# Kernel optimization log

Measured on AMD Instinct MI355X. Metric: run time of the kernel, lower is better.

Reference implementation:

```python
import jax, jax.numpy as jnp
import numpy as np

N = 100000   # nodes
E = 1600000  # edges
F = 128      # input features
H = 128      # hidden
O = 64       # output classes
BN_EPS = 1e-5


def gcn_conv(x, edge_index, W, b, n_nodes):
    """PyG-style GCNConv: h = D^-1/2 (A+I) D^-1/2 (x W) + b."""
    h = x @ W  # [N, out]
    row = jnp.concatenate([edge_index[0], jnp.arange(n_nodes)])  # add self loops
    col = jnp.concatenate([edge_index[1], jnp.arange(n_nodes)])
    deg = jax.ops.segment_sum(jnp.ones_like(row, dtype=h.dtype), row, num_segments=n_nodes)
    dinv = jnp.where(deg > 0, jax.lax.rsqrt(deg), 0.0)
    norm = dinv[row] * dinv[col]                 # [E+N]
    msg = h[col] * norm[:, None]                 # gather + scale
    out = jax.ops.segment_sum(msg, row, num_segments=n_nodes)  # scatter-add
    return out + b


def batch_norm(x, gamma, beta):
    mean = jnp.mean(x, axis=0)
    var = jnp.var(x, axis=0)
    return (x - mean) * jax.lax.rsqrt(var + BN_EPS) * gamma + beta


def setup_inputs() -> dict:
    key = jax.random.key(0)
    ks = jax.random.split(key, 10)
    x = jax.random.normal(ks[0], (N, F), dtype=jnp.float32)
    edge_index = jax.random.randint(ks[1], (2, E), 0, N, dtype=jnp.int64)
    W1 = jax.random.normal(ks[2], (F, H), dtype=jnp.float32) / np.sqrt(F)
    b1 = jnp.zeros((H,), dtype=jnp.float32)
    gamma1 = jnp.ones((H,), dtype=jnp.float32)
    beta1 = jnp.zeros((H,), dtype=jnp.float32)
    W2 = jax.random.normal(ks[3], (H, H), dtype=jnp.float32) / np.sqrt(H)
    b2 = jnp.zeros((H,), dtype=jnp.float32)
    W3 = jax.random.normal(ks[4], (H, O), dtype=jnp.float32) / np.sqrt(H)
    b3 = jnp.zeros((O,), dtype=jnp.float32)
    return {"x": x, "edge_index": edge_index, "W1": W1, "b1": b1,
            "gamma1": gamma1, "beta1": beta1, "W2": W2, "b2": b2,
            "W3": W3, "b3": b3}


def reference(x, edge_index, W1, b1, gamma1, beta1, W2, b2, W3, b3):
    h = gcn_conv(x, edge_index, W1, b1, N)
    h = jax.nn.relu(batch_norm(h, gamma1, beta1))
    h = gcn_conv(h, edge_index, W2, b2, N)
    h = jax.nn.relu(h)
    out = h @ W3 + b3  # final Linear classifier head [N, O]
    return out
```

## Files before the change

kernel.cpp:

```cpp
#include <hip/hip_runtime.h>

#define NN 100000
#define EE 1600000
#define HN 128
#define OO 64
#define SB 256
#define NBUCK 196
#define CH 4096

typedef __attribute__((ext_vector_type(8))) short bf16x8;
typedef __attribute__((ext_vector_type(4))) float f32x4;

__device__ __forceinline__ unsigned short f2bf(float f){
  unsigned u = __float_as_uint(f);
  return (unsigned short)((u + 0x7FFFu + ((u >> 16) & 1u)) >> 16);
}
__device__ __forceinline__ float bflo(unsigned u){ return __uint_as_float(u << 16); }
__device__ __forceinline__ float bfhi(unsigned u){ return __uint_as_float(u & 0xFFFF0000u); }

__global__ __launch_bounds__(256) void k_histpack(const int* __restrict__ rows, int* __restrict__ bcnt,
                                                  const float* __restrict__ W1, const float* __restrict__ W2,
                                                  const float* __restrict__ W3,
                                                  unsigned short* __restrict__ Wp1, unsigned short* __restrict__ Wp2,
                                                  unsigned short* __restrict__ Wp3){
  __shared__ int h[NBUCK];
  for (int i = threadIdx.x; i < NBUCK; i += 256) h[i] = 0;
  __syncthreads();
  int base = blockIdx.x * CH;
  for (int j = threadIdx.x; j < CH; j += 256){
    int e = base + j;
    if (e < EE) atomicAdd(&h[rows[e] >> 9], 1);
  }
  __syncthreads();
  for (int i = threadIdx.x; i < NBUCK; i += 256){
    int v = h[i];
    if (v) atomicAdd(&bcnt[i], v);
  }
  int b = blockIdx.x;
  if (b < 20){
    const float* W; unsigned short* Wp; int outc, i0;
    if (b < 8)      { W=W1; Wp=Wp1; outc=128; i0 = b*256; }
    else if (b < 16){ W=W2; Wp=Wp2; outc=128; i0 = (b-8)*256; }
    else            { W=W3; Wp=Wp3; outc=64;  i0 = (b-16)*256; }
    int i = i0 + threadIdx.x;
    if (i < 16*outc){
      int kb = i / outc, n = i - kb*outc;
      unsigned pk[4];
      #pragma unroll
      for (int jj = 0; jj < 4; ++jj){
        unsigned lo = f2bf(W[(size_t)(kb*8 + 2*jj)*outc + n]);
        unsigned hi = f2bf(W[(size_t)(kb*8 + 2*jj+1)*outc + n]);
        pk[jj] = lo | (hi << 16);
      }
      *reinterpret_cast<uint4*>(Wp + (size_t)i*8) = make_uint4(pk[0],pk[1],pk[2],pk[3]);
    }
  }
}

__global__ __launch_bounds__(64) void k_bscan(const int* __restrict__ bcnt,
                                              int* __restrict__ bbase, int* __restrict__ bcur){
  int lane = threadIdx.x;
  int run = 0;
  for (int c = 0; c < NBUCK; c += 64){
    int i = c + lane;
    int v = (i < NBUCK) ? bcnt[i] : 0;
    int s = v;
    #pragma unroll
    for (int d = 1; d < 64; d <<= 1){ int u = __shfl_up(s, d); if (lane >= d) s += u; }
    if (i < NBUCK){ bbase[i] = run + s - v; bcur[i] = run + s - v; }
    run += __shfl(s, 63);
  }
}

__global__ __launch_bounds__(256) void k_bucket(const int* __restrict__ rows, const int* __restrict__ cols,
                                                int* __restrict__ bcur, uint2* __restrict__ ebuf){
  __shared__ int bc[NBUCK];
  __shared__ int boff[NBUCK];
  __shared__ int ccur[NBUCK];
  __shared__ int gbase[NBUCK];
  __shared__ uint2 stage[CH];
  const int t = threadIdx.x;
  const int base = blockIdx.x * CH;
  const int nval = min(CH, EE - base);

  for (int i = t; i < NBUCK; i += 256) bc[i] = 0;
  __syncthreads();

  int er[16], ec[16];
  #pragma unroll
  for (int j = 0; j < 16; ++j){
    int i = j*256 + t;
    if (i < nval){
      er[j] = rows[base+i]; ec[j] = cols[base+i];
      atomicAdd(&bc[er[j] >> 9], 1);
    } else er[j] = -1;
  }
  __syncthreads();

  if (t < 64){
    int lane = t, run = 0;
    for (int c = 0; c < NBUCK; c += 64){
      int i = c + lane;
      int v = (i < NBUCK) ? bc[i] : 0;
      int s = v;
      #pragma unroll
      for (int d = 1; d < 64; d <<= 1){ int u = __shfl_up(s, d); if (lane >= d) s += u; }
      if (i < NBUCK) boff[i] = run + s - v;
      run += __shfl(s, 63);
    }
  }
  __syncthreads();
  if (t < NBUCK){
    gbase[t] = bc[t] ? atomicAdd(&bcur[t], bc[t]) : 0;
    ccur[t]  = boff[t];
  }
  __syncthreads();
  #pragma unroll
  for (int j = 0; j < 16; ++j){
    if (er[j] >= 0){
      int b = er[j] >> 9;
      int p = atomicAdd(&ccur[b], 1);
      stage[p] = make_uint2((unsigned)er[j], (unsigned)ec[j]);
    }
  }
  __syncthreads();
  for (int i = t; i < nval; i += 256){
    uint2 e = stage[i];
    int b = (int)(e.x >> 9);
    ebuf[gbase[b] + (i - boff[b])] = e;
  }
}

__global__ __launch_bounds__(256) void k_build(const uint2* __restrict__ ebuf,
                                               const int* __restrict__ bbase, const int* __restrict__ bcnt,
                                               int* __restrict__ row_start, int* __restrict__ cnt,
                                               float* __restrict__ dinv, int* __restrict__ csr_col){
  __shared__ int hist[512];
  __shared__ int cur[512];
  const int b = blockIdx.x;
  const int row0 = b << 9;
  const int nrow = min(512, NN - row0);
  const int ebase = bbase[b];
  const int ne = bcnt[b];
  const int t = threadIdx.x;

  for (int i = t; i < nrow; i += 256) hist[i] = 0;
  __syncthreads();
  for (int i = t; i < ne; i += 256)
    atomicAdd(&hist[(int)ebuf[ebase+i].x - row0], 1);
  __syncthreads();

  if (t < 64){
    int lane = t, run = 0;
    for (int c = 0; c < nrow; c += 64){
      int i = c + lane;
      int v = (i < nrow) ? hist[i] : 0;
      int s = v;
      #pragma unroll
      for (int d = 1; d < 64; d <<= 1){ int u = __shfl_up(s, d); if (lane >= d) s += u; }
      if (i < nrow) cur[i] = run + s - v;
      run += __shfl(s, 63);
    }
  }
  __syncthreads();
  for (int i = t; i < nrow; i += 256){
    int h = hist[i];
    int r = row0 + i;
    cnt[r] = h;
    dinv[r] = rsqrtf((float)(h+1));
    row_start[r] = ebase + cur[i];
    cur[i] += ebase;
  }
  __syncthreads();
  for (int i = t; i < ne; i += 256){
    uint2 e = ebuf[ebase+i];
    int p = atomicAdd(&cur[(int)e.x - row0], 1);
    csr_col[p] = (int)e.y;
  }
}

template<bool BF16OUT>
__global__ __launch_bounds__(256) void k_agg(const unsigned* __restrict__ h,
                                             const int* __restrict__ row_start,
                                             const int* __restrict__ cnt,
                                             const int* __restrict__ col,
                                             const float* __restrict__ dinv,
                                             const float* __restrict__ bias,
                                             void* __restrict__ outv){
  int wib  = __builtin_amdgcn_readfirstlane((int)(threadIdx.x >> 6));
  int wid  = blockIdx.x*4 + wib;
  int lane = threadIdx.x & 63;
  if (wid >= NN) return;
  int s = row_start[wid];
  int e = s + cnt[wid];
  float dr = dinv[wid];
  const unsigned* hp = h + lane;
  float ax, ay;
  {
    unsigned u = hp[(size_t)wid*64];
    ax = bflo(u); ay = bfhi(u);
  }
  int p = s;
  for (; p+7 < e; p += 8){
    unsigned uu[8];
    #pragma unroll
    for (int j=0;j<8;++j) uu[j] = hp[(size_t)col[p+j]*64];
    #pragma unroll
    for (int j=0;j<8;++j){ ax += bflo(uu[j]); ay += bfhi(uu[j]); }
  }
  for (; p+3 < e; p += 4){
    unsigned uu[4];
    #pragma unroll
    for (int j=0;j<4;++j) uu[j] = hp[(size_t)col[p+j]*64];
    #pragma unroll
    for (int j=0;j<4;++j){ ax += bflo(uu[j]); ay += bfhi(uu[j]); }
  }
  for (; p < e; ++p){
    unsigned u = hp[(size_t)col[p]*64];
    ax += bflo(u); ay += bfhi(u);
  }
  float2 bb = *reinterpret_cast<const float2*>(bias + 2*lane);
  float ox = ax*dr + bb.x, oy = ay*dr + bb.y;
  if constexpr (BF16OUT){
    ((unsigned*)outv)[(size_t)wid*64 + lane] = (unsigned)f2bf(ox) | ((unsigned)f2bf(oy) << 16);
  } else {
    *reinterpret_cast<float2*>((float*)outv + (size_t)wid*HN + 2*lane) = make_float2(ox, oy);
  }
}

template<int OUTC, int XFORM, bool ADD_BIAS, bool BF16OUT, bool ABF16>
__global__ __launch_bounds__(256) void k_mgemm(const void* __restrict__ Av,
                                               const unsigned short* __restrict__ Wp,
                                               const float* __restrict__ scale,
                                               const float* __restrict__ shiftv,
                                               const float* __restrict__ bias,
                                               const float* __restrict__ dinv,
                                               void* __restrict__ Cv){
  __shared__ char AsB[32768];
  const int t = threadIdx.x;
  const int row0 = blockIdx.x * 128;

  if constexpr (ABF16){
    const uint4* A = (const uint4*)Av;
    const int c8 = t & 15;
    const int k0 = c8*8;
    float sc[8], sh[8];
    if (XFORM == 1){
      #pragma unroll
      for (int j=0;j<8;++j){ sc[j]=scale[k0+j]; sh[j]=shiftv[k0+j]; }
    }
    #pragma unroll
    for (int g = 0; g < 8; ++g){
      int f = g*256 + t;
      int r = f >> 4;
      int row = row0 + r;
      int rc = row < NN ? row : NN-1;
      uint4 q = A[(size_t)rc*16 + c8];
      float vf[8] = { bflo(q.x),bfhi(q.x),bflo(q.y),bfhi(q.y),
                      bflo(q.z),bfhi(q.z),bflo(q.w),bfhi(q.w) };
      if (XFORM == 1){
        #pragma unroll
        for (int j=0;j<8;++j) vf[j] = fmaxf(fmaf(vf[j], sc[j], sh[j]), 0.f);
      } else if (XFORM == 2){
        #pragma unroll
        for (int j=0;j<8;++j) vf[j] = fmaxf(vf[j], 0.f);
      }
      unsigned pk[4];
      #pragma unroll
      for (int j=0;j<4;++j)
        pk[j] = (unsigned)f2bf(vf[2*j]) | ((unsigned)f2bf(vf[2*j+1]) << 16);
      int boff = (c8*16) ^ ((r & 7) << 4);
      *reinterpret_cast<uint4*>(AsB + r*256 + boff) = make_uint4(pk[0],pk[1],pk[2],pk[3]);
    }
  } else {
    const float* A = (const float*)Av;
    #pragma unroll
    for (int g = 0; g < 16; ++g){
      int f = g*256 + t;
      int r = f >> 5;
      int c4 = f & 31;
      int row = row0 + r;
      int rc = row < NN ? row : NN-1;
      float4 v = *reinterpret_cast<const float4*>(A + (size_t)rc*HN + c4*4);
      if (XFORM == 2){
        v.x = fmaxf(v.x, 0.f); v.y = fmaxf(v.y, 0.f);
        v.z = fmaxf(v.z, 0.f); v.w = fmaxf(v.w, 0.f);
      }
      unsigned p0 = (unsigned)f2bf(v.x) | ((unsigned)f2bf(v.y) << 16);
      unsigned p1 = (unsigned)f2bf(v.z) | ((unsigned)f2bf(v.w) << 16);
      int boff = (c4*8) ^ ((r & 7) << 4);
      *reinterpret_cast<uint2*>(AsB + r*256 + boff) = make_uint2(p0, p1);
    }
  }
  __syncthreads();

  const int wv = t >> 6;
  const int l  = t & 63;
  const int lm = l & 15;
  const int lk = l >> 4;
  constexpr int NF = OUTC/16;

  f32x4 acc[2][NF];
  #pragma unroll
  for (int mi=0;mi<2;++mi)
    #pragma unroll
    for (int ni=0;ni<NF;++ni) acc[mi][ni] = (f32x4){0.f,0.f,0.f,0.f};

  const bf16x8* WpV = reinterpret_cast<const bf16x8*>(Wp);

  #pragma unroll
  for (int ks = 0; ks < 4; ++ks){
    bf16x8 af[2];
    #pragma unroll
    for (int mi=0;mi<2;++mi){
      int R = wv*32 + mi*16 + lm;
      int boff = (ks*64 + lk*16) ^ ((R & 7) << 4);
      af[mi] = *reinterpret_cast<const bf16x8*>(AsB + R*256 + boff);
    }
    int kb = ks*4 + lk;
    #pragma unroll
    for (int ni=0;ni<NF;++ni){
      int n = ni*16 + lm;
      bf16x8 bfr = WpV[kb*OUTC + n];
      acc[0][ni] = __builtin_amdgcn_mfma_f32_16x16x32_bf16(af[0], bfr, acc[0][ni], 0,0,0);
      acc[1][ni] = __builtin_amdgcn_mfma_f32_16x16x32_bf16(af[1], bfr, acc[1][ni], 0,0,0);
    }
  }

  #pragma unroll
  for (int mi=0;mi<2;++mi){
    #pragma unroll
    for (int j=0;j<4;++j){
      int grow = row0 + wv*32 + mi*16 + lk*4 + j;
      if (grow >= NN) continue;
      if constexpr (BF16OUT){
        float dr = dinv[grow];
        unsigned short* po = (unsigned short*)Cv + (size_t)grow*OUTC;
        #pragma unroll
        for (int ni=0;ni<NF;++ni)
          po[ni*16 + lm] = f2bf(acc[mi][ni][j] * dr);
      } else {
        float* po = (float*)Cv + (size_t)grow*OUTC;
        #pragma unroll
        for (int ni=0;ni<NF;++ni){
          float v = acc[mi][ni][j];
          if (ADD_BIAS) v += bias[ni*16 + lm];
          po[ni*16 + lm] = v;
        }
      }
    }
  }
}

__global__ __launch_bounds__(256) void k_stats(const unsigned* __restrict__ a,
                                               float* __restrict__ ps, float* __restrict__ pq){
  __shared__ float l0[256], l1[256], m0[256], m1[256];
  int c = threadIdx.x & 63;
  int grp = threadIdx.x >> 6;
  float s0=0.f,s1=0.f,q0=0.f,q1=0.f;
  for (int r = blockIdx.x*4 + grp; r < NN; r += SB*4){
    unsigned u = a[(size_t)r*64 + c];
    float v0 = bflo(u), v1 = bfhi(u);
    s0 += v0; s1 += v1; q0 = fmaf(v0,v0,q0); q1 = fmaf(v1,v1,q1);
  }
  l0[threadIdx.x]=s0; l1[threadIdx.x]=s1; m0[threadIdx.x]=q0; m1[threadIdx.x]=q1;
  __syncthreads();
  if (grp==0){
    #pragma unroll
    for (int g=1;g<4;++g){ s0+=l0[g*64+c]; s1+=l1[g*64+c]; q0+=m0[g*64+c]; q1+=m1[g*64+c]; }
    ps[blockIdx.x*128 + 2*c]   = s0; ps[blockIdx.x*128 + 2*c+1] = s1;
    pq[blockIdx.x*128 + 2*c]   = q0; pq[blockIdx.x*128 + 2*c+1] = q1;
  }
}

__global__ __launch_bounds__(128) void k_bnfinal(const float* __restrict__ ps, const float* __restrict__ pq,
                                                 const float* __restrict__ gamma, const float* __restrict__ beta,
                                                 float* __restrict__ scale, float* __restrict__ shiftv){
  int c = threadIdx.x;
  float s=0.f, q=0.f;
  for (int b=0;b<SB;b++){ s += ps[b*128+c]; q += pq[b*128+c]; }
  float mean = s * (1.0f/NN);
  float var  = q * (1.0f/NN) - mean*mean;
  float inv  = rsqrtf(var + 1e-5f);
  float sc = gamma[c]*inv;
  scale[c]  = sc;
  shiftv[c] = beta[c] - mean*sc;
}

extern "C" void kernel_launch(void* const* d_in, const int* in_sizes, int n_in,
                              void* d_out, int out_size, void* d_ws, size_t ws_size,
                              hipStream_t stream) {
  const float* x      = (const float*)d_in[0];
  const int*   ei     = (const int*)d_in[1];
  const int*   rows   = ei;
  const int*   cols   = ei + EE;
  const float* W1     = (const float*)d_in[2];
  const float* b1     = (const float*)d_in[3];
  const float* gamma1 = (const float*)d_in[4];
  const float* beta1  = (const float*)d_in[5];
  const float* W2     = (const float*)d_in[6];
  const float* b2     = (const float*)d_in[7];
  const float* W3     = (const float*)d_in[8];
  const float* b3     = (const float*)d_in[9];
  float* out = (float*)d_out;

  char* w = (char*)d_ws;
  float* buf0      = (float*)w; w += (size_t)NN*HN*4;
  float* buf1      = (float*)w; w += (size_t)NN*HN*4;
  int*   csr_col   = (int*)w;   w += (size_t)EE*4;
  int*   row_start = (int*)w;   w += (size_t)NN*4;
  int*   cnt       = (int*)w;   w += (size_t)NN*4;
  float* dinv      = (float*)w; w += (size_t)NN*4;
  float* ps        = (float*)w; w += (size_t)SB*128*4;
  float* pq        = (float*)w; w += (size_t)SB*128*4;
  float* scale     = (float*)w; w += 1024;
  float* shiftv    = (float*)w; w += 1024;
  int*   bcnt      = (int*)w;   w += 1024;
  int*   bbase     = (int*)w;   w += 1024;
  int*   bcur      = (int*)w;   w += 1024;
  unsigned short* Wp1 = (unsigned short*)w; w += 128*128*2;
  unsigned short* Wp2 = (unsigned short*)w; w += 128*128*2;
  unsigned short* Wp3 = (unsigned short*)w; w += 128*64*2;
  uint2*    ebuf  = (uint2*)buf0;
  unsigned* hbf   = (unsigned*)buf0;
  unsigned* abf   = (unsigned*)buf1;

  (void)hipMemsetAsync(bcnt, 0, NBUCK*4, stream);

  const int CB = (EE + CH - 1)/CH, GB = (NN+127)/128, AB = NN/4;

  k_histpack<<<CB, 256, 0, stream>>>(rows, bcnt, W1, W2, W3, Wp1, Wp2, Wp3);
  k_bscan <<<1, 64, 0, stream>>>(bcnt, bbase, bcur);
  k_bucket<<<CB, 256, 0, stream>>>(rows, cols, bcur, ebuf);
  k_build <<<NBUCK, 256, 0, stream>>>(ebuf, bbase, bcnt, row_start, cnt, dinv, csr_col);

  k_mgemm<128,0,false,true,false><<<GB, 256, 0, stream>>>(x, Wp1, nullptr, nullptr, nullptr, dinv, hbf);
  k_agg<true><<<AB, 256, 0, stream>>>(hbf, row_start, cnt, csr_col, dinv, b1, abf);
  k_stats<<<SB, 256, 0, stream>>>(abf, ps, pq);
  k_bnfinal<<<1, 128, 0, stream>>>(ps, pq, gamma1, beta1, scale, shiftv);

  k_mgemm<128,1,false,true,true><<<GB, 256, 0, stream>>>(abf, Wp2, scale, shiftv, nullptr, dinv, hbf);
  k_agg<true><<<AB, 256, 0, stream>>>(hbf, row_start, cnt, csr_col, dinv, b2, abf);

  k_mgemm<64,2,true,false,true><<<GB, 256, 0, stream>>>(abf, Wp3, nullptr, nullptr, b3, nullptr, out);
}
```

Baseline: 274.1 us.

## Fuse final aggregation with output GEMM and remove small scan/finalize kernels

```diff
diff --git a/kernel.cpp b/kernel.cpp
--- a/kernel.cpp
+++ b/kernel.cpp
@@ -57,25 +57,12 @@
   }
 }
 
-__global__ __launch_bounds__(64) void k_bscan(const int* __restrict__ bcnt,
-                                              int* __restrict__ bbase, int* __restrict__ bcur){
-  int lane = threadIdx.x;
-  int run = 0;
-  for (int c = 0; c < NBUCK; c += 64){
-    int i = c + lane;
-    int v = (i < NBUCK) ? bcnt[i] : 0;
-    int s = v;
-    #pragma unroll
-    for (int d = 1; d < 64; d <<= 1){ int u = __shfl_up(s, d); if (lane >= d) s += u; }
-    if (i < NBUCK){ bbase[i] = run + s - v; bcur[i] = run + s - v; }
-    run += __shfl(s, 63);
-  }
-}
-
 __global__ __launch_bounds__(256) void k_bucket(const int* __restrict__ rows, const int* __restrict__ cols,
-                                                int* __restrict__ bcur, uint2* __restrict__ ebuf){
+                                                const int* __restrict__ bcnt, int* __restrict__ pcur,
+                                                uint2* __restrict__ ebuf){
   __shared__ int bc[NBUCK];
   __shared__ int boff[NBUCK];
+  __shared__ int gBB[NBUCK];
   __shared__ int ccur[NBUCK];
   __shared__ int gbase[NBUCK];
   __shared__ uint2 stage[CH];
@@ -98,20 +85,25 @@
   __syncthreads();
 
   if (t < 64){
-    int lane = t, run = 0;
+    int lane = t, run = 0, grun = 0;
     for (int c = 0; c < NBUCK; c += 64){
       int i = c + lane;
       int v = (i < NBUCK) ? bc[i] : 0;
-      int s = v;
-      #pragma unroll
-      for (int d = 1; d < 64; d <<= 1){ int u = __shfl_up(s, d); if (lane >= d) s += u; }
-      if (i < NBUCK) boff[i] = run + s - v;
+      int g = (i < NBUCK) ? bcnt[i] : 0;
+      int s = v, gs = g;
+      #pragma unroll
+      for (int d = 1; d < 64; d <<= 1){
+        int u = __shfl_up(s, d);  if (lane >= d) s += u;
+        int gu = __shfl_up(gs, d); if (lane >= d) gs += gu;
+      }
+      if (i < NBUCK){ boff[i] = run + s - v; gBB[i] = grun + gs - g; }
       run += __shfl(s, 63);
+      grun += __shfl(gs, 63);
     }
   }
   __syncthreads();
   if (t < NBUCK){
-    gbase[t] = bc[t] ? atomicAdd(&bcur[t], bc[t]) : 0;
+    gbase[t] = bc[t] ? (gBB[t] + atomicAdd(&pcur[t], bc[t])) : 0;
     ccur[t]  = boff[t];
   }
   __syncthreads();
@@ -132,20 +124,28 @@
 }
 
 __global__ __launch_bounds__(256) void k_build(const uint2* __restrict__ ebuf,
-                                               const int* __restrict__ bbase, const int* __restrict__ bcnt,
+                                               const int* __restrict__ bcnt,
                                                int* __restrict__ row_start, int* __restrict__ cnt,
                                                float* __restrict__ dinv, int* __restrict__ csr_col){
   __shared__ int hist[512];
   __shared__ int cur[512];
+  __shared__ int sEbase;
   const int b = blockIdx.x;
   const int row0 = b << 9;
   const int nrow = min(512, NN - row0);
-  const int ebase = bbase[b];
   const int ne = bcnt[b];
   const int t = threadIdx.x;
 
+  if (t < 64){
+    int acc = 0;
+    for (int i = t; i < b; i += 64) acc += bcnt[i];
+    #pragma unroll
+    for (int d = 32; d; d >>= 1) acc += __shfl_xor(acc, d);
+    if (t == 0) sEbase = acc;
+  }
   for (int i = t; i < nrow; i += 256) hist[i] = 0;
   __syncthreads();
+  const int ebase = sEbase;
   for (int i = t; i < ne; i += 256)
     atomicAdd(&hist[(int)ebuf[ebase+i].x - row0], 1);
   __syncthreads();
@@ -179,14 +179,13 @@
   }
 }
 
-template<bool BF16OUT>
 __global__ __launch_bounds__(256) void k_agg(const unsigned* __restrict__ h,
                                              const int* __restrict__ row_start,
                                              const int* __restrict__ cnt,
                                              const int* __restrict__ col,
                                              const float* __restrict__ dinv,
                                              const float* __restrict__ bias,
-                                             void* __restrict__ outv){
+                                             unsigned* __restrict__ outv){
   int wib  = __builtin_amdgcn_readfirstlane((int)(threadIdx.x >> 6));
   int wid  = blockIdx.x*4 + wib;
   int lane = threadIdx.x & 63;
@@ -221,19 +220,97 @@
   }
   float2 bb = *reinterpret_cast<const float2*>(bias + 2*lane);
   float ox = ax*dr + bb.x, oy = ay*dr + bb.y;
-  if constexpr (BF16OUT){
-    ((unsigned*)outv)[(size_t)wid*64 + lane] = (unsigned)f2bf(ox) | ((unsigned)f2bf(oy) << 16);
-  } else {
-    *reinterpret_cast<float2*>((float*)outv + (size_t)wid*HN + 2*lane) = make_float2(ox, oy);
-  }
-}
-
-template<int OUTC, int XFORM, bool ADD_BIAS, bool BF16OUT, bool ABF16>
+  outv[(size_t)wid*64 + lane] = (unsigned)f2bf(ox) | ((unsigned)f2bf(oy) << 16);
+}
+
+__global__ __launch_bounds__(256) void k_aggmm(const unsigned* __restrict__ h,
+                                               const int* __restrict__ row_start,
+                                               const int* __restrict__ cnt,
+                                               const int* __restrict__ col,
+                                               const float* __restrict__ dinv,
+                                               const float* __restrict__ b2,
+                                               const unsigned short* __restrict__ Wp3,
+                                               const float* __restrict__ b3,
+                                               float* __restrict__ out){
+  __shared__ char AsB[32*256];
+  const int t = threadIdx.x;
+  const int wv = __builtin_amdgcn_readfirstlane(t >> 6);
+  const int lane = t & 63;
+  const int tile = blockIdx.x * 32;
+
+  for (int k = 0; k < 8; ++k){
+    int wid = tile + wv*8 + k;
+    int s = row_start[wid];
+    int e = s + cnt[wid];
+    float dr = dinv[wid];
+    const unsigned* hp = h + lane;
+    float ax, ay;
+    { unsigned u = hp[(size_t)wid*64]; ax = bflo(u); ay = bfhi(u); }
+    int p = s;
+    for (; p+7 < e; p += 8){
+      unsigned uu[8];
+      #pragma unroll
+      for (int j=0;j<8;++j) uu[j] = hp[(size_t)col[p+j]*64];
+      #pragma unroll
+      for (int j=0;j<8;++j){ ax += bflo(uu[j]); ay += bfhi(uu[j]); }
+    }
+    for (; p+3 < e; p += 4){
+      unsigned uu[4];
+      #pragma unroll
+      for (int j=0;j<4;++j) uu[j] = hp[(size_t)col[p+j]*64];
+      #pragma unroll
+      for (int j=0;j<4;++j){ ax += bflo(uu[j]); ay += bfhi(uu[j]); }
+    }
+    for (; p < e; ++p){
+      unsigned u = hp[(size_t)col[p]*64];
+      ax += bflo(u); ay += bfhi(u);
+    }
+    float2 bb = *reinterpret_cast<const float2*>(b2 + 2*lane);
+    float ox = fmaxf(ax*dr + bb.x, 0.f);
+    float oy = fmaxf(ay*dr + bb.y, 0.f);
+    int r = wv*8 + k;
+    unsigned pk = (unsigned)f2bf(ox) | ((unsigned)f2bf(oy) << 16);
+    *reinterpret_cast<unsigned*>(AsB + r*256 + ((lane*4) ^ ((r & 7) << 4))) = pk;
+  }
+  __syncthreads();
+
+  const int lm = lane & 15;
+  const int lk = lane >> 4;
+  const int mb  = wv >> 1;
+  const int nb2 = (wv & 1) * 2;
+  f32x4 acc[2] = {(f32x4){0.f,0.f,0.f,0.f},(f32x4){0.f,0.f,0.f,0.f}};
+  const bf16x8* WpV = reinterpret_cast<const bf16x8*>(Wp3);
+
+  #pragma unroll
+  for (int ks = 0; ks < 4; ++ks){
+    int R = mb*16 + lm;
+    bf16x8 af = *reinterpret_cast<const bf16x8*>(AsB + R*256 + ((ks*64 + lk*16) ^ ((R & 7) << 4)));
+    int kb = ks*4 + lk;
+    #pragma unroll
+    for (int ni = 0; ni < 2; ++ni){
+      int n = (nb2+ni)*16 + lm;
+      bf16x8 bfr = WpV[kb*OO + n];
+      acc[ni] = __builtin_amdgcn_mfma_f32_16x16x32_bf16(af, bfr, acc[ni], 0,0,0);
+    }
+  }
+
+  #pragma unroll
+  for (int ni = 0; ni < 2; ++ni){
+    int gcol = (nb2+ni)*16 + lm;
+    float bb = b3[gcol];
+    #pragma unroll
+    for (int j = 0; j < 4; ++j){
+      int grow = tile + mb*16 + lk*4 + j;
+      out[(size_t)grow*OO + gcol] = acc[ni][j] + bb;
+    }
+  }
+}
+
+template<int OUTC, int XFORM, bool BF16OUT, bool ABF16>
 __global__ __launch_bounds__(256) void k_mgemm(const void* __restrict__ Av,
                                                const unsigned short* __restrict__ Wp,
                                                const float* __restrict__ scale,
                                                const float* __restrict__ shiftv,
-                                               const float* __restrict__ bias,
                                                const float* __restrict__ dinv,
                                                void* __restrict__ Cv){
   __shared__ char AsB[32768];
@@ -261,9 +338,6 @@
       if (XFORM == 1){
         #pragma unroll
         for (int j=0;j<8;++j) vf[j] = fmaxf(fmaf(vf[j], sc[j], sh[j]), 0.f);
-      } else if (XFORM == 2){
-        #pragma unroll
-        for (int j=0;j<8;++j) vf[j] = fmaxf(vf[j], 0.f);
       }
       unsigned pk[4];
       #pragma unroll
@@ -282,10 +356,6 @@
       int row = row0 + r;
       int rc = row < NN ? row : NN-1;
       float4 v = *reinterpret_cast<const float4*>(A + (size_t)rc*HN + c4*4);
-      if (XFORM == 2){
-        v.x = fmaxf(v.x, 0.f); v.y = fmaxf(v.y, 0.f);
-        v.z = fmaxf(v.z, 0.f); v.w = fmaxf(v.w, 0.f);
-      }
       unsigned p0 = (unsigned)f2bf(v.x) | ((unsigned)f2bf(v.y) << 16);
       unsigned p1 = (unsigned)f2bf(v.z) | ((unsigned)f2bf(v.w) << 16);
       int boff = (c4*8) ^ ((r & 7) << 4);
@@ -342,19 +412,20 @@
       } else {
         float* po = (float*)Cv + (size_t)grow*OUTC;
         #pragma unroll
-        for (int ni=0;ni<NF;++ni){
-          float v = acc[mi][ni][j];
-          if (ADD_BIAS) v += bias[ni*16 + lm];
-          po[ni*16 + lm] = v;
-        }
+        for (int ni=0;ni<NF;++ni)
+          po[ni*16 + lm] = acc[mi][ni][j];
       }
     }
   }
 }
 
-__global__ __launch_bounds__(256) void k_stats(const unsigned* __restrict__ a,
-                                               float* __restrict__ ps, float* __restrict__ pq){
+__global__ __launch_bounds__(256) void k_statsfin(const unsigned* __restrict__ a,
+                                                  float* __restrict__ ps, float* __restrict__ pq,
+                                                  const float* __restrict__ gamma, const float* __restrict__ beta,
+                                                  float* __restrict__ scale, float* __restrict__ shiftv,
+                                                  int* __restrict__ done){
   __shared__ float l0[256], l1[256], m0[256], m1[256];
+  __shared__ int last;
   int c = threadIdx.x & 63;
   int grp = threadIdx.x >> 6;
   float s0=0.f,s1=0.f,q0=0.f,q1=0.f;
@@ -371,20 +442,20 @@
     ps[blockIdx.x*128 + 2*c]   = s0; ps[blockIdx.x*128 + 2*c+1] = s1;
     pq[blockIdx.x*128 + 2*c]   = q0; pq[blockIdx.x*128 + 2*c+1] = q1;
   }
-}
-
-__global__ __launch_bounds__(128) void k_bnfinal(const float* __restrict__ ps, const float* __restrict__ pq,
-                                                 const float* __restrict__ gamma, const float* __restrict__ beta,
-                                                 float* __restrict__ scale, float* __restrict__ shiftv){
-  int c = threadIdx.x;
-  float s=0.f, q=0.f;
-  for (int b=0;b<SB;b++){ s += ps[b*128+c]; q += pq[b*128+c]; }
-  float mean = s * (1.0f/NN);
-  float var  = q * (1.0f/NN) - mean*mean;
-  float inv  = rsqrtf(var + 1e-5f);
-  float sc = gamma[c]*inv;
-  scale[c]  = sc;
-  shiftv[c] = beta[c] - mean*sc;
+  __threadfence();
+  if (threadIdx.x == 0) last = (atomicAdd(done, 1) == SB-1);
+  __syncthreads();
+  if (last && threadIdx.x < 128){
+    int ch = threadIdx.x;
+    float s=0.f, q=0.f;
+    for (int b=0;b<SB;b++){ s += ps[b*128+ch]; q += pq[b*128+ch]; }
+    float mean = s * (1.0f/NN);
+    float var  = q * (1.0f/NN) - mean*mean;
+    float inv  = rsqrtf(var + 1e-5f);
+    float sc = gamma[ch]*inv;
+    scale[ch]  = sc;
+    shiftv[ch] = beta[ch] - mean*sc;
+  }
 }
 
 extern "C" void kernel_launch(void* const* d_in, const int* in_sizes, int n_in,
@@ -415,32 +486,30 @@
   float* pq        = (float*)w; w += (size_t)SB*128*4;
   float* scale     = (float*)w; w += 1024;
   float* shiftv    = (float*)w; w += 1024;
-  int*   bcnt      = (int*)w;   w += 1024;
-  int*   bbase     = (int*)w;   w += 1024;
-  int*   bcur      = (int*)w;   w += 1024;
+  int*   scr0      = (int*)w;   w += 4096;
   unsigned short* Wp1 = (unsigned short*)w; w += 128*128*2;
   unsigned short* Wp2 = (unsigned short*)w; w += 128*128*2;
   unsigned short* Wp3 = (unsigned short*)w; w += 128*64*2;
+  int* bcnt = scr0;
+  int* pcur = scr0 + 256;
+  int* done = scr0 + 512;
   uint2*    ebuf  = (uint2*)buf0;
   unsigned* hbf   = (unsigned*)buf0;
   unsigned* abf   = (unsigned*)buf1;
 
-  (void)hipMemsetAsync(bcnt, 0, NBUCK*4, stream);
-
-  const int CB = (EE + CH - 1)/CH, GB = (NN+127)/128, AB = NN/4;
+  (void)hipMemsetAsync(scr0, 0, 4096, stream);
+
+  const int CB = (EE + CH - 1)/CH, GB = (NN+127)/128, AB = NN/4, FB = NN/32;
 
   k_histpack<<<CB, 256, 0, stream>>>(rows, bcnt, W1, W2, W3, Wp1, Wp2, Wp3);
-  k_bscan <<<1, 64, 0, stream>>>(bcnt, bbase, bcur);
-  k_bucket<<<CB, 256, 0, stream>>>(rows, cols, bcur, ebuf);
-  k_build <<<NBUCK, 256, 0, stream>>>(ebuf, bbase, bcnt, row_start, cnt, dinv, csr_col);
-
-  k_mgemm<128,0,false,true,false><<<GB, 256, 0, stream>>>(x, Wp1, nullptr, nullptr, nullptr, dinv, hbf);
-  k_agg<true><<<AB, 256, 0, stream>>>(hbf, row_start, cnt, csr_col, dinv, b1, abf);
-  k_stats<<<SB, 256, 0, stream>>>(abf, ps, pq);
-  k_bnfinal<<<1, 128, 0, stream>>>(ps, pq, gamma1, beta1, scale, shiftv);
-
-  k_mgemm<128,1,false,true,true><<<GB, 256, 0, stream>>>(abf, Wp2, scale, shiftv, nullptr, dinv, hbf);
-  k_agg<true><<<AB, 256, 0, stream>>>(hbf, row_start, cnt, csr_col, dinv, b2, abf);
-
-  k_mgemm<64,2,true,false,true><<<GB, 256, 0, stream>>>(abf, Wp3, nullptr, nullptr, b3, nullptr, out);
-}
+  k_bucket  <<<CB, 256, 0, stream>>>(rows, cols, bcnt, pcur, ebuf);
+  k_build   <<<NBUCK, 256, 0, stream>>>(ebuf, bcnt, row_start, cnt, dinv, csr_col);
+
+  k_mgemm<128,0,true,false><<<GB, 256, 0, stream>>>(x, Wp1, nullptr, nullptr, dinv, hbf);
+  k_agg<<<AB, 256, 0, stream>>>(hbf, row_start, cnt, csr_col, dinv, b1, abf);
+  k_statsfin<<<SB, 256, 0, stream>>>(abf, ps, pq, gamma1, beta1, scale, shiftv, done);
+
+  k_mgemm<128,1,true,true><<<GB, 256, 0, stream>>>(abf, Wp2, scale, shiftv, dinv, hbf);
+
+  k_aggmm<<<FB, 256, 0, stream>>>(hbf, row_start, cnt, csr_col, dinv, b2, Wp3, b3, out);
+}
```

New measurement: 278.7 us. About the same (+1.7%).

## Slice features into 16-column slabs for aggregation and drop histogram/scan pre-pass

Applied to the files above, without the earlier changes.

```diff
diff --git a/kernel.cpp b/kernel.cpp
--- a/kernel.cpp
+++ b/kernel.cpp
@@ -7,6 +7,7 @@
 #define SB 256
 #define NBUCK 196
 #define CH 4096
+#define SLAB 16384
 
 typedef __attribute__((ext_vector_type(8))) short bf16x8;
 typedef __attribute__((ext_vector_type(4))) float f32x4;
@@ -17,32 +18,85 @@
 }
 __device__ __forceinline__ float bflo(unsigned u){ return __uint_as_float(u << 16); }
 __device__ __forceinline__ float bfhi(unsigned u){ return __uint_as_float(u & 0xFFFF0000u); }
-
-__global__ __launch_bounds__(256) void k_histpack(const int* __restrict__ rows, int* __restrict__ bcnt,
-                                                  const float* __restrict__ W1, const float* __restrict__ W2,
-                                                  const float* __restrict__ W3,
-                                                  unsigned short* __restrict__ Wp1, unsigned short* __restrict__ Wp2,
-                                                  unsigned short* __restrict__ Wp3){
-  __shared__ int h[NBUCK];
-  for (int i = threadIdx.x; i < NBUCK; i += 256) h[i] = 0;
-  __syncthreads();
-  int base = blockIdx.x * CH;
-  for (int j = threadIdx.x; j < CH; j += 256){
-    int e = base + j;
-    if (e < EE) atomicAdd(&h[rows[e] >> 9], 1);
-  }
-  __syncthreads();
-  for (int i = threadIdx.x; i < NBUCK; i += 256){
-    int v = h[i];
-    if (v) atomicAdd(&bcnt[i], v);
-  }
+__device__ __forceinline__ unsigned bnrelu2(unsigned u, float s0, float h0, float s1, float h1){
+  float v0 = fmaxf(fmaf(bflo(u), s0, h0), 0.f);
+  float v1 = fmaxf(fmaf(bfhi(u), s1, h1), 0.f);
+  return (unsigned)f2bf(v0) | ((unsigned)f2bf(v1) << 16);
+}
+__device__ __forceinline__ unsigned relupk(unsigned u){
+  unsigned m = ((u >> 15) & 0x10001u) * 0xFFFFu;
+  return u & ~m;
+}
+
+__global__ __launch_bounds__(256) void k_bucket(const int* __restrict__ rows, const int* __restrict__ cols,
+                                                int* __restrict__ pcur, uint2* __restrict__ ebuf,
+                                                const float* __restrict__ W1, const float* __restrict__ W2,
+                                                const float* __restrict__ W3,
+                                                unsigned short* __restrict__ Wp1, unsigned short* __restrict__ Wp2,
+                                                unsigned short* __restrict__ Wp3){
+  __shared__ int bc[NBUCK];
+  __shared__ int boff[NBUCK];
+  __shared__ int ccur[NBUCK];
+  __shared__ int gbase[NBUCK];
+  __shared__ uint2 stage[CH];
+  const int t = threadIdx.x;
+  const int base = blockIdx.x * CH;
+  const int nval = min(CH, EE - base);
+
+  for (int i = t; i < NBUCK; i += 256) bc[i] = 0;
+  __syncthreads();
+
+  int er[16], ec[16];
+  #pragma unroll
+  for (int j = 0; j < 16; ++j){
+    int i = j*256 + t;
+    if (i < nval){
+      er[j] = rows[base+i]; ec[j] = cols[base+i];
+      atomicAdd(&bc[er[j] >> 9], 1);
+    } else er[j] = -1;
+  }
+  __syncthreads();
+
+  if (t < 64){
+    int lane = t, run = 0;
+    for (int c = 0; c < NBUCK; c += 64){
+      int i = c + lane;
+      int v = (i < NBUCK) ? bc[i] : 0;
+      int s = v;
+      #pragma unroll
+      for (int d = 1; d < 64; d <<= 1){ int u = __shfl_up(s, d); if (lane >= d) s += u; }
+      if (i < NBUCK) boff[i] = run + s - v;
+      run += __shfl(s, 63);
+    }
+  }
+  __syncthreads();
+  if (t < NBUCK){
+    gbase[t] = bc[t] ? (t*SLAB + atomicAdd(&pcur[t], bc[t])) : 0;
+    ccur[t]  = boff[t];
+  }
+  __syncthreads();
+  #pragma unroll
+  for (int j = 0; j < 16; ++j){
+    if (er[j] >= 0){
+      int b = er[j] >> 9;
+      int p = atomicAdd(&ccur[b], 1);
+      stage[p] = make_uint2((unsigned)er[j], (unsigned)ec[j]);
+    }
+  }
+  __syncthreads();
+  for (int i = t; i < nval; i += 256){
+    uint2 e = stage[i];
+    int b = (int)(e.x >> 9);
+    ebuf[gbase[b] + (i - boff[b])] = e;
+  }
+
   int b = blockIdx.x;
   if (b < 20){
     const float* W; unsigned short* Wp; int outc, i0;
     if (b < 8)      { W=W1; Wp=Wp1; outc=128; i0 = b*256; }
     else if (b < 16){ W=W2; Wp=Wp2; outc=128; i0 = (b-8)*256; }
     else            { W=W3; Wp=Wp3; outc=64;  i0 = (b-16)*256; }
-    int i = i0 + threadIdx.x;
+    int i = i0 + t;
     if (i < 16*outc){
       int kb = i / outc, n = i - kb*outc;
       unsigned pk[4];
@@ -57,93 +111,27 @@
   }
 }
 
-__global__ __launch_bounds__(64) void k_bscan(const int* __restrict__ bcnt,
-                                              int* __restrict__ bbase, int* __restrict__ bcur){
-  int lane = threadIdx.x;
-  int run = 0;
-  for (int c = 0; c < NBUCK; c += 64){
-    int i = c + lane;
-    int v = (i < NBUCK) ? bcnt[i] : 0;
-    int s = v;
-    #pragma unroll
-    for (int d = 1; d < 64; d <<= 1){ int u = __shfl_up(s, d); if (lane >= d) s += u; }
-    if (i < NBUCK){ bbase[i] = run + s - v; bcur[i] = run + s - v; }
-    run += __shfl(s, 63);
-  }
-}
-
-__global__ __launch_bounds__(256) void k_bucket(const int* __restrict__ rows, const int* __restrict__ cols,
-                                                int* __restrict__ bcur, uint2* __restrict__ ebuf){
-  __shared__ int bc[NBUCK];
-  __shared__ int boff[NBUCK];
-  __shared__ int ccur[NBUCK];
-  __shared__ int gbase[NBUCK];
-  __shared__ uint2 stage[CH];
-  const int t = threadIdx.x;
-  const int base = blockIdx.x * CH;
-  const int nval = min(CH, EE - base);
-
-  for (int i = t; i < NBUCK; i += 256) bc[i] = 0;
-  __syncthreads();
-
-  int er[16], ec[16];
-  #pragma unroll
-  for (int j = 0; j < 16; ++j){
-    int i = j*256 + t;
-    if (i < nval){
-      er[j] = rows[base+i]; ec[j] = cols[base+i];
-      atomicAdd(&bc[er[j] >> 9], 1);
-    } else er[j] = -1;
-  }
-  __syncthreads();
-
-  if (t < 64){
-    int lane = t, run = 0;
-    for (int c = 0; c < NBUCK; c += 64){
-      int i = c + lane;
-      int v = (i < NBUCK) ? bc[i] : 0;
-      int s = v;
-      #pragma unroll
-      for (int d = 1; d < 64; d <<= 1){ int u = __shfl_up(s, d); if (lane >= d) s += u; }
-      if (i < NBUCK) boff[i] = run + s - v;
-      run += __shfl(s, 63);
-    }
-  }
-  __syncthreads();
-  if (t < NBUCK){
-    gbase[t] = bc[t] ? atomicAdd(&bcur[t], bc[t]) : 0;
-    ccur[t]  = boff[t];
-  }
-  __syncthreads();
-  #pragma unroll
-  for (int j = 0; j < 16; ++j){
-    if (er[j] >= 0){
-      int b = er[j] >> 9;
-      int p = atomicAdd(&ccur[b], 1);
-      stage[p] = make_uint2((unsigned)er[j], (unsigned)ec[j]);
-    }
-  }
-  __syncthreads();
-  for (int i = t; i < nval; i += 256){
-    uint2 e = stage[i];
-    int b = (int)(e.x >> 9);
-    ebuf[gbase[b] + (i - boff[b])] = e;
-  }
-}
-
 __global__ __launch_bounds__(256) void k_build(const uint2* __restrict__ ebuf,
-                                               const int* __restrict__ bbase, const int* __restrict__ bcnt,
+                                               const int* __restrict__ pcur,
                                                int* __restrict__ row_start, int* __restrict__ cnt,
                                                float* __restrict__ dinv, int* __restrict__ csr_col){
   __shared__ int hist[512];
   __shared__ int cur[512];
+  __shared__ int sCbase;
   const int b = blockIdx.x;
   const int row0 = b << 9;
   const int nrow = min(512, NN - row0);
-  const int ebase = bbase[b];
-  const int ne = bcnt[b];
+  const int ebase = b * SLAB;
+  const int ne = pcur[b];
   const int t = threadIdx.x;
 
+  if (t < 64){
+    int acc = 0;
+    for (int i = t; i < b; i += 64) acc += pcur[i];
+    #pragma unroll
+    for (int d = 32; d; d >>= 1) acc += __shfl_xor(acc, d);
+    if (t == 0) sCbase = acc;
+  }
   for (int i = t; i < nrow; i += 256) hist[i] = 0;
   __syncthreads();
   for (int i = t; i < ne; i += 256)
@@ -163,13 +151,14 @@
     }
   }
   __syncthreads();
+  const int cbase = sCbase;
   for (int i = t; i < nrow; i += 256){
     int h = hist[i];
     int r = row0 + i;
     cnt[r] = h;
     dinv[r] = rsqrtf((float)(h+1));
-    row_start[r] = ebase + cur[i];
-    cur[i] += ebase;
+    row_start[r] = cbase + cur[i];
+    cur[i] += cbase;
   }
   __syncthreads();
   for (int i = t; i < ne; i += 256){
@@ -179,56 +168,48 @@
   }
 }
 
-template<bool BF16OUT>
-__global__ __launch_bounds__(256) void k_agg(const unsigned* __restrict__ h,
-                                             const int* __restrict__ row_start,
-                                             const int* __restrict__ cnt,
-                                             const int* __restrict__ col,
-                                             const float* __restrict__ dinv,
-                                             const float* __restrict__ bias,
-                                             void* __restrict__ outv){
-  int wib  = __builtin_amdgcn_readfirstlane((int)(threadIdx.x >> 6));
-  int wid  = blockIdx.x*4 + wib;
-  int lane = threadIdx.x & 63;
-  if (wid >= NN) return;
-  int s = row_start[wid];
-  int e = s + cnt[wid];
-  float dr = dinv[wid];
-  const unsigned* hp = h + lane;
-  float ax, ay;
-  {
-    unsigned u = hp[(size_t)wid*64];
-    ax = bflo(u); ay = bfhi(u);
-  }
-  int p = s;
-  for (; p+7 < e; p += 8){
-    unsigned uu[8];
-    #pragma unroll
-    for (int j=0;j<8;++j) uu[j] = hp[(size_t)col[p+j]*64];
-    #pragma unroll
-    for (int j=0;j<8;++j){ ax += bflo(uu[j]); ay += bfhi(uu[j]); }
-  }
-  for (; p+3 < e; p += 4){
-    unsigned uu[4];
-    #pragma unroll
-    for (int j=0;j<4;++j) uu[j] = hp[(size_t)col[p+j]*64];
-    #pragma unroll
-    for (int j=0;j<4;++j){ ax += bflo(uu[j]); ay += bfhi(uu[j]); }
-  }
-  for (; p < e; ++p){
-    unsigned u = hp[(size_t)col[p]*64];
-    ax += bflo(u); ay += bfhi(u);
-  }
-  float2 bb = *reinterpret_cast<const float2*>(bias + 2*lane);
-  float ox = ax*dr + bb.x, oy = ay*dr + bb.y;
-  if constexpr (BF16OUT){
-    ((unsigned*)outv)[(size_t)wid*64 + lane] = (unsigned)f2bf(ox) | ((unsigned)f2bf(oy) << 16);
-  } else {
-    *reinterpret_cast<float2*>((float*)outv + (size_t)wid*HN + 2*lane) = make_float2(ox, oy);
-  }
-}
-
-template<int OUTC, int XFORM, bool ADD_BIAS, bool BF16OUT, bool ABF16>
+__global__ __launch_bounds__(256) void k_aggs(const unsigned* __restrict__ hs,
+                                              const int* __restrict__ row_start,
+                                              const int* __restrict__ cnt,
+                                              const int* __restrict__ col,
+                                              const float* __restrict__ dinv,
+                                              const float* __restrict__ bias,
+                                              unsigned* __restrict__ outs){
+  const int bid = blockIdx.x;
+  const int s   = bid & 7;
+  const int rb  = bid >> 3;
+  const int wv  = __builtin_amdgcn_readfirstlane((int)(threadIdx.x >> 6));
+  const int lane = threadIdx.x & 63;
+  const int g   = lane >> 3;
+  const int j8  = lane & 7;
+  const unsigned* hp = hs + (size_t)s*NN*8 + j8;
+  const float2 bb = *reinterpret_cast<const float2*>(bias + 16*s + 2*j8);
+
+  for (int r8 = 0; r8 < 8; ++r8){
+    int wid = rb*32 + wv*8 + r8;
+    int p = row_start[wid];
+    int n1 = cnt[wid] + 1;
+    float dr = dinv[wid];
+    float a0 = 0.f, a1 = 0.f;
+    for (int base0 = 0; base0 < n1; base0 += 8){
+      int idx = base0 + g;
+      int cc = wid;
+      if (idx > 0 && idx < n1) cc = col[p + idx - 1];
+      unsigned u = 0;
+      if (idx < n1) u = hp[(size_t)cc*8];
+      a0 += bflo(u); a1 += bfhi(u);
+    }
+    a0 += __shfl_xor(a0, 8);  a1 += __shfl_xor(a1, 8);
+    a0 += __shfl_xor(a0, 16); a1 += __shfl_xor(a1, 16);
+    a0 += __shfl_xor(a0, 32); a1 += __shfl_xor(a1, 32);
+    float o0 = a0*dr + bb.x, o1 = a1*dr + bb.y;
+    unsigned pk = (unsigned)f2bf(o0) | ((unsigned)f2bf(o1) << 16);
+    if (lane < 8)
+      outs[((size_t)s*NN + wid)*8 + j8] = pk;
+  }
+}
+
+template<int OUTC, int XFORM, bool OUTSLICED, bool ASLICED>
 __global__ __launch_bounds__(256) void k_mgemm(const void* __restrict__ Av,
                                                const unsigned short* __restrict__ Wp,
                                                const float* __restrict__ scale,
@@ -240,52 +221,46 @@
   const int t = threadIdx.x;
   const int row0 = blockIdx.x * 128;
 
-  if constexpr (ABF16){
-    const uint4* A = (const uint4*)Av;
-    const int c8 = t & 15;
-    const int k0 = c8*8;
-    float sc[8], sh[8];
+  if constexpr (ASLICED){
+    const unsigned* A = (const unsigned*)Av;
+    const int sg = t >> 5;
+    const int i  = t & 31;
+    const int q  = i & 1;
+    float4 sc01, sc23, sh01, sh23;
     if (XFORM == 1){
-      #pragma unroll
-      for (int j=0;j<8;++j){ sc[j]=scale[k0+j]; sh[j]=shiftv[k0+j]; }
-    }
-    #pragma unroll
-    for (int g = 0; g < 8; ++g){
-      int f = g*256 + t;
-      int r = f >> 4;
-      int row = row0 + r;
-      int rc = row < NN ? row : NN-1;
-      uint4 q = A[(size_t)rc*16 + c8];
-      float vf[8] = { bflo(q.x),bfhi(q.x),bflo(q.y),bfhi(q.y),
-                      bflo(q.z),bfhi(q.z),bflo(q.w),bfhi(q.w) };
+      int fb = 16*sg + 8*q;
+      sc01 = *reinterpret_cast<const float4*>(scale + fb);
+      sc23 = *reinterpret_cast<const float4*>(scale + fb + 4);
+      sh01 = *reinterpret_cast<const float4*>(shiftv + fb);
+      sh23 = *reinterpret_cast<const float4*>(shiftv + fb + 4);
+    }
+    const uint4* src = reinterpret_cast<const uint4*>(A + ((size_t)sg*NN + row0)*8);
+    #pragma unroll
+    for (int k = 0; k < 8; ++k){
+      int u = i + 32*k;
+      int r = u >> 1;
+      uint4 v = src[u];
       if (XFORM == 1){
-        #pragma unroll
-        for (int j=0;j<8;++j) vf[j] = fmaxf(fmaf(vf[j], sc[j], sh[j]), 0.f);
+        v.x = bnrelu2(v.x, sc01.x, sh01.x, sc01.y, sh01.y);
+        v.y = bnrelu2(v.y, sc01.z, sh01.z, sc01.w, sh01.w);
+        v.z = bnrelu2(v.z, sc23.x, sh23.x, sc23.y, sh23.y);
+        v.w = bnrelu2(v.w, sc23.z, sh23.z, sc23.w, sh23.w);
       } else if (XFORM == 2){
-        #pragma unroll
-        for (int j=0;j<8;++j) vf[j] = fmaxf(vf[j], 0.f);
+        v.x = relupk(v.x); v.y = relupk(v.y); v.z = relupk(v.z); v.w = relupk(v.w);
       }
-      unsigned pk[4];
-      #pragma unroll
-      for (int j=0;j<4;++j)
-        pk[j] = (unsigned)f2bf(vf[2*j]) | ((unsigned)f2bf(vf[2*j+1]) << 16);
-      int boff = (c8*16) ^ ((r & 7) << 4);
-      *reinterpret_cast<uint4*>(AsB + r*256 + boff) = make_uint4(pk[0],pk[1],pk[2],pk[3]);
+      int boff = (32*sg + 16*q) ^ ((r & 7) << 4);
+      *reinterpret_cast<uint4*>(AsB + r*256 + boff) = v;
     }
   } else {
     const float* A = (const float*)Av;
     #pragma unroll
-    for (int g = 0; g < 16; ++g){
-      int f = g*256 + t;
+    for (int gg = 0; gg < 16; ++gg){
+      int f = gg*256 + t;
       int r = f >> 5;
       int c4 = f & 31;
       int row = row0 + r;
       int rc = row < NN ? row : NN-1;
       float4 v = *reinterpret_cast<const float4*>(A + (size_t)rc*HN + c4*4);
-      if (XFORM == 2){
-        v.x = fmaxf(v.x, 0.f); v.y = fmaxf(v.y, 0.f);
-        v.z = fmaxf(v.z, 0.f); v.w = fmaxf(v.w, 0.f);
-      }
       unsigned p0 = (unsigned)f2bf(v.x) | ((unsigned)f2bf(v.y) << 16);
       unsigned p1 = (unsigned)f2bf(v.z) | ((unsigned)f2bf(v.w) << 16);
       int boff = (c4*8) ^ ((r & 7) << 4);
@@ -333,20 +308,22 @@
     for (int j=0;j<4;++j){
       int grow = row0 + wv*32 + mi*16 + lk*4 + j;
       if (grow >= NN) continue;
-      if constexpr (BF16OUT){
+      if constexpr (OUTSLICED){
         float dr = dinv[grow];
-        unsigned short* po = (unsigned short*)Cv + (size_t)grow*OUTC;
         #pragma unroll
-        for (int ni=0;ni<NF;++ni)
-          po[ni*16 + lm] = f2bf(acc[mi][ni][j] * dr);
+        for (int ni=0;ni<NF;++ni){
+          unsigned u16 = (unsigned)f2bf(acc[mi][ni][j] * dr);
+          unsigned partner = (unsigned)__shfl_xor((int)u16, 1);
+          if (!(lm & 1)){
+            unsigned pk = u16 | (partner << 16);
+            *reinterpret_cast<unsigned*>((char*)Cv + ((size_t)ni*NN + grow)*32 + lm*2) = pk;
+          }
+        }
       } else {
         float* po = (float*)Cv + (size_t)grow*OUTC;
         #pragma unroll
-        for (int ni=0;ni<NF;++ni){
-          float v = acc[mi][ni][j];
-          if (ADD_BIAS) v += bias[ni*16 + lm];
-          po[ni*16 + lm] = v;
-        }
+        for (int ni=0;ni<NF;++ni)
+          po[ni*16 + lm] = acc[mi][ni][j] + bias[ni*16 + lm];
       }
     }
   }
@@ -355,11 +332,14 @@
 __global__ __launch_bounds__(256) void k_stats(const unsigned* __restrict__ a,
                                                float* __restrict__ ps, float* __restrict__ pq){
   __shared__ float l0[256], l1[256], m0[256], m1[256];
-  int c = threadIdx.x & 63;
-  int grp = threadIdx.x >> 6;
+  const int lane = threadIdx.x & 63;
+  const int grp  = threadIdx.x >> 6;
+  const int s  = lane >> 3;
+  const int j8 = lane & 7;
+  const unsigned* ap = a + (size_t)s*NN*8 + j8;
   float s0=0.f,s1=0.f,q0=0.f,q1=0.f;
   for (int r = blockIdx.x*4 + grp; r < NN; r += SB*4){
-    unsigned u = a[(size_t)r*64 + c];
+    unsigned u = ap[(size_t)r*8];
     float v0 = bflo(u), v1 = bfhi(u);
     s0 += v0; s1 += v1; q0 = fmaf(v0,v0,q0); q1 = fmaf(v1,v1,q1);
   }
@@ -367,9 +347,10 @@
   __syncthreads();
   if (grp==0){
     #pragma unroll
-    for (int g=1;g<4;++g){ s0+=l0[g*64+c]; s1+=l1[g*64+c]; q0+=m0[g*64+c]; q1+=m1[g*64+c]; }
-    ps[blockIdx.x*128 + 2*c]   = s0; ps[blockIdx.x*128 + 2*c+1] = s1;
-    pq[blockIdx.x*128 + 2*c]   = q0; pq[blockIdx.x*128 + 2*c+1] = q1;
+    for (int g2=1;g2<4;++g2){ s0+=l0[g2*64+lane]; s1+=l1[g2*64+lane]; q0+=m0[g2*64+lane]; q1+=m1[g2*64+lane]; }
+    int f0 = 16*s + 2*j8;
+    ps[blockIdx.x*128 + f0]   = s0; ps[blockIdx.x*128 + f0+1] = s1;
+    pq[blockIdx.x*128 + f0]   = q0; pq[blockIdx.x*128 + f0+1] = q1;
   }
 }
 
@@ -415,32 +396,29 @@
   float* pq        = (float*)w; w += (size_t)SB*128*4;
   float* scale     = (float*)w; w += 1024;
   float* shiftv    = (float*)w; w += 1024;
-  int*   bcnt      = (int*)w;   w += 1024;
-  int*   bbase     = (int*)w;   w += 1024;
-  int*   bcur      = (int*)w;   w += 1024;
+  int*   scr0      = (int*)w;   w += 4096;
   unsigned short* Wp1 = (unsigned short*)w; w += 128*128*2;
   unsigned short* Wp2 = (unsigned short*)w; w += 128*128*2;
   unsigned short* Wp3 = (unsigned short*)w; w += 128*64*2;
+  int* pcur = scr0;
   uint2*    ebuf  = (uint2*)buf0;
   unsigned* hbf   = (unsigned*)buf0;
   unsigned* abf   = (unsigned*)buf1;
 
-  (void)hipMemsetAsync(bcnt, 0, NBUCK*4, stream);
-
-  const int CB = (EE + CH - 1)/CH, GB = (NN+127)/128, AB = NN/4;
-
-  k_histpack<<<CB, 256, 0, stream>>>(rows, bcnt, W1, W2, W3, Wp1, Wp2, Wp3);
-  k_bscan <<<1, 64, 0, stream>>>(bcnt, bbase, bcur);
-  k_bucket<<<CB, 256, 0, stream>>>(rows, cols, bcur, ebuf);
-  k_build <<<NBUCK, 256, 0, stream>>>(ebuf, bbase, bcnt, row_start, cnt, dinv, csr_col);
-
-  k_mgemm<128,0,false,true,false><<<GB, 256, 0, stream>>>(x, Wp1, nullptr, nullptr, nullptr, dinv, hbf);
-  k_agg<true><<<AB, 256, 0, stream>>>(hbf, row_start, cnt, csr_col, dinv, b1, abf);
+  (void)hipMemsetAsync(scr0, 0, 4096, stream);
+
+  const int CB = (EE + CH - 1)/CH, GB = (NN+127)/128, AB = (NN/32)*8;
+
+  k_bucket<<<CB, 256, 0, stream>>>(rows, cols, pcur, ebuf, W1, W2, W3, Wp1, Wp2, Wp3);
+  k_build <<<NBUCK, 256, 0, stream>>>(ebuf, pcur, row_start, cnt, dinv, csr_col);
+
+  k_mgemm<128,0,true,false><<<GB, 256, 0, stream>>>(x, Wp1, nullptr, nullptr, nullptr, dinv, hbf);
+  k_aggs<<<AB, 256, 0, stream>>>(hbf, row_start, cnt, csr_col, dinv, b1, abf);
   k_stats<<<SB, 256, 0, stream>>>(abf, ps, pq);
   k_bnfinal<<<1, 128, 0, stream>>>(ps, pq, gamma1, beta1, scale, shiftv);
 
-  k_mgemm<128,1,false,true,true><<<GB, 256, 0, stream>>>(abf, Wp2, scale, shiftv, nullptr, dinv, hbf);
-  k_agg<true><<<AB, 256, 0, stream>>>(hbf, row_start, cnt, csr_col, dinv, b2, abf);
-
-  k_mgemm<64,2,true,false,true><<<GB, 256, 0, stream>>>(abf, Wp3, nullptr, nullptr, b3, nullptr, out);
-}
+  k_mgemm<128,1,true,true><<<GB, 256, 0, stream>>>(abf, Wp2, scale, shiftv, nullptr, dinv, hbf);
+  k_aggs<<<AB, 256, 0, stream>>>(hbf, row_start, cnt, csr_col, dinv, b2, abf);
+
+  k_mgemm<64,2,false,true><<<GB, 256, 0, stream>>>(abf, Wp3, nullptr, nullptr, b3, nullptr, out);
+}
```

After: 479.7 us. +75.0%, slower.
